# Optimization experiments

Measured on AMD Instinct MI355X. Metric: run time of the kernel, lower is better.

The kernel has to match this reference:

```python
import jax, jax.numpy as jnp
import numpy as np

B, T, C, H = 4, 2048, 1024, 16
HD = C // H  # head_dim = 64


def setup_inputs() -> dict:
    key = jax.random.key(0)
    k1, k2, k3 = jax.random.split(key, 3)
    x = jax.random.normal(k1, (B, T, C), dtype=jnp.float32)
    # nn.Linear weights are [out, in]; we store transposed [in, out] for x @ W
    w_qkv = jax.random.normal(k2, (C, 3 * C), dtype=jnp.float32) * (1.0 / np.sqrt(C))
    w_proj = jax.random.normal(k3, (C, C), dtype=jnp.float32) * (1.0 / np.sqrt(C))
    return {"x": x, "w_qkv": w_qkv, "w_proj": w_proj}


def reference(x, w_qkv, w_proj):
    Bs, Ts, Cs = x.shape
    qkv = x @ w_qkv  # [B,T,3C]
    q, k, v = jnp.split(qkv, 3, axis=-1)

    def split_heads(t):
        return t.reshape(Bs, Ts, H, HD).transpose(0, 2, 1, 3)  # [B,H,T,HD]

    q, k, v = split_heads(q), split_heads(k), split_heads(v)
    scale = 1.0 / np.sqrt(HD)
    scores = jnp.einsum('bhqd,bhkd->bhqk', q, k) * scale  # [B,H,T,T]
    causal = jnp.tril(jnp.ones((Ts, Ts), dtype=bool))
    scores = jnp.where(causal, scores, -jnp.inf)
    weights = jax.nn.softmax(scores, axis=-1)
    out = jnp.einsum('bhqk,bhkd->bhqd', weights, v)  # [B,H,T,HD]
    out = out.transpose(0, 2, 1, 3).reshape(Bs, Ts, Cs)
    return out @ w_proj
```

## Files before the change

kernel.cpp:

```cpp
#include <hip/hip_runtime.h>
#include <stdint.h>


typedef __attribute__((ext_vector_type(8))) short bf16x8;
typedef __attribute__((ext_vector_type(4))) float f32x4;

#define MFMA(a, b, c) __builtin_amdgcn_mfma_f32_16x16x32_bf16((a), (b), (c), 0, 0, 0)

#define NB 4
#define NT 2048
#define NC 1024
#define NH 16
#define HD 64
#define SCALE_Q 0.18033688011112042f

__device__ __forceinline__ short f2bf(float f) {
  union { float fv; uint32_t u; } v; v.fv = f;
  uint32_t u = v.u;
  uint32_t r = (u + 0x7fffu + ((u >> 16) & 1u)) >> 16;
  return (short)(r & 0xffffu);
}

__device__ __forceinline__ void gl_lds16(const void* g, void* l) {
  __builtin_amdgcn_global_load_lds(
      (const __attribute__((address_space(1))) void*)g,
      (__attribute__((address_space(3))) void*)l, 16, 0, 0);
}


__global__ void cast_f32_bf16(const float* __restrict__ src, short* __restrict__ dst, int n8) {
  int i = blockIdx.x * blockDim.x + threadIdx.x;
  if (i >= n8) return;
  const float4* s4 = (const float4*)src;
  float4 a = s4[2 * i], b = s4[2 * i + 1];
  bf16x8 o;
  o[0] = f2bf(a.x); o[1] = f2bf(a.y); o[2] = f2bf(a.z); o[3] = f2bf(a.w);
  o[4] = f2bf(b.x); o[5] = f2bf(b.y); o[6] = f2bf(b.z); o[7] = f2bf(b.w);
  *(bf16x8*)&dst[8 * i] = o;
}

__global__ void transpose_cast(const float* __restrict__ src, short* __restrict__ dst,
                               int R, int Cc) {
  __shared__ float tile[64][65];
  int tid = threadIdx.x;
  int c0 = blockIdx.x * 64;
  int r0 = blockIdx.y * 64;
  int lr = tid >> 4;
  int lc = (tid & 15) * 4;
#pragma unroll
  for (int i = 0; i < 4; i++) {
    int rr = lr + i * 16;
    float4 v = *(const float4*)&src[(size_t)(r0 + rr) * Cc + c0 + lc];
    tile[rr][lc + 0] = v.x; tile[rr][lc + 1] = v.y;
    tile[rr][lc + 2] = v.z; tile[rr][lc + 3] = v.w;
  }
  __syncthreads();
  int oc = tid >> 2;
  int seg = (tid & 3) * 16;
  bf16x8 o0, o1;
#pragma unroll
  for (int u = 0; u < 8; u++) o0[u] = f2bf(tile[seg + u][oc]);
#pragma unroll
  for (int u = 0; u < 8; u++) o1[u] = f2bf(tile[seg + 8 + u][oc]);
  size_t base = (size_t)(c0 + oc) * R + r0 + seg;
  *(bf16x8*)&dst[base] = o0;
  *(bf16x8*)&dst[base + 8] = o1;
}


__global__ __launch_bounds__(256, 2)
void gemm_bt_kernel(const short* __restrict__ A, const short* __restrict__ BT,
                    int N, int K, int nbx, int mode,
                    short* __restrict__ q, short* __restrict__ kk, short* __restrict__ vT,
                    float* __restrict__ f_out) {
  __shared__ short sA[128 * 64];
  __shared__ short sB[128 * 64];
  const int tid = threadIdx.x;
  const int lane = tid & 63;
  const int w = tid >> 6;
  const int quad = lane >> 4;
  const int r = lane & 15;

  const int bid = blockIdx.x;
  const int xcd = bid & 7;
  const int local = bid >> 3;
  const int mloc = local / nbx, nloc = local - mloc * nbx;
  const int bm0 = (xcd * 8 + mloc) * 128;
  const int bn0 = nloc * 128;

  const int wm = (w >> 1) * 64;
  const int wn = (w & 1) * 64;
  const int sel = (mode == 0) ? (bn0 >> 10) : 3;
  const bool swapped = (sel != 2);

  f32x4 acc[4][4];
#pragma unroll
  for (int i = 0; i < 4; i++)
#pragma unroll
    for (int j = 0; j < 4; j++) acc[i][j] = (f32x4){0.f, 0.f, 0.f, 0.f};

  for (int kb = 0; kb < K; kb += 64) {
    __syncthreads();
#pragma unroll
    for (int j2 = 0; j2 < 4; j2++) {
      int idx = (w * 4 + j2) * 64 + lane;
      int row = idx >> 3, ch = idx & 7;
      int g = ch ^ (row & 7);
      gl_lds16(A + (size_t)(bm0 + row) * K + kb + g * 8, (char*)sA + idx * 16);
      gl_lds16(BT + (size_t)(bn0 + row) * K + kb + g * 8, (char*)sB + idx * 16);
    }
    __syncthreads();
#pragma unroll
    for (int c = 0; c < 2; c++) {
      bf16x8 af[4], bfr[4];
#pragma unroll
      for (int i = 0; i < 4; i++) {
        const int sw = ((c << 2) + quad) ^ (r & 7);
        af[i]  = *(const bf16x8*)&sA[(wm + i * 16 + r) * 64 + sw * 8];
        bfr[i] = *(const bf16x8*)&sB[(wn + i * 16 + r) * 64 + sw * 8];
      }
      if (swapped) {
#pragma unroll
        for (int i = 0; i < 4; i++)
#pragma unroll
          for (int j = 0; j < 4; j++)
            acc[i][j] = MFMA(bfr[j], af[i], acc[i][j]);
      } else {
#pragma unroll
        for (int i = 0; i < 4; i++)
#pragma unroll
          for (int j = 0; j < 4; j++)
            acc[i][j] = MFMA(af[i], bfr[j], acc[i][j]);
      }
    }
  }

  if (mode == 1) {
#pragma unroll
    for (int i = 0; i < 4; i++) {
      const int m = bm0 + wm + i * 16 + r;
#pragma unroll
      for (int j = 0; j < 4; j++) {
        const int nf = bn0 + wn + j * 16 + quad * 4;
        *(f32x4*)&f_out[(size_t)m * N + nf] = acc[i][j];
      }
    }
  } else if (sel == 2) {
#pragma unroll
    for (int j = 0; j < 4; j++) {
      const int n = bn0 + wn + j * 16 + r;
      const int d = n & 63, h = (n & 1023) >> 6;
#pragma unroll
      for (int i = 0; i < 4; i++) {
        const int t0 = bm0 + wm + i * 16 + quad * 4;
        const int bh = (t0 >> 11) * NH + h;
        uint32_t p0 = (uint16_t)f2bf(acc[i][j][0]) | ((uint32_t)(uint16_t)f2bf(acc[i][j][1]) << 16);
        uint32_t p1 = (uint16_t)f2bf(acc[i][j][2]) | ((uint32_t)(uint16_t)f2bf(acc[i][j][3]) << 16);
        *(uint2*)&vT[((size_t)bh * HD + d) * NT + (t0 & 2047)] = make_uint2(p0, p1);
      }
    }
  } else {
    short* dst = (sel == 0) ? q : kk;
    const float scl = (sel == 0) ? SCALE_Q : 1.0f;
#pragma unroll
    for (int i = 0; i < 4; i++) {
      const int t = bm0 + wm + i * 16 + r;
      const int bb = (t >> 11) * NH;
      const int tt = t & 2047;
#pragma unroll
      for (int j = 0; j < 4; j++) {
        const int nf = bn0 + wn + j * 16 + quad * 4;
        const int rem = nf & 1023, h = rem >> 6, d0 = rem & 63;
        uint32_t p0 = (uint16_t)f2bf(acc[i][j][0] * scl) | ((uint32_t)(uint16_t)f2bf(acc[i][j][1] * scl) << 16);
        uint32_t p1 = (uint16_t)f2bf(acc[i][j][2] * scl) | ((uint32_t)(uint16_t)f2bf(acc[i][j][3] * scl) << 16);
        *(uint2*)&dst[((size_t)(bb + h) * NT + tt) * HD + d0] = make_uint2(p0, p1);
      }
    }
  }
}


__global__ __launch_bounds__(256, 3)
void attn_kernel(const short* __restrict__ Q, const short* __restrict__ Kg,
                 const short* __restrict__ VT, short* __restrict__ Og) {
  __shared__ short sK[128 * 64];
  __shared__ short sV[64 * 128];
  __shared__ short sP[4][16 * 136];
  const int tid = threadIdx.x;
  const int lane = tid & 63;
  const int w = tid >> 6;
  const int quad = lane >> 4;
  const int r = lane & 15;

  const int n = blockIdx.x;
  const int xcd = n & 7;
  const int slot = n >> 3;
  const int bh = xcd * 8 + (slot & 7);
  const int band = 15 - (slot >> 3);
  const int ntile = band + 1;

  const short* Qb  = Q  + (size_t)bh * NT * HD;
  const short* Kb  = Kg + (size_t)bh * NT * HD;
  const short* VTb = VT + (size_t)bh * HD * NT;

  const int q0 = band * 128 + w * 32;

  bf16x8 bQ[2][2];
#pragma unroll
  for (int mi = 0; mi < 2; mi++) {
    const size_t qrow = ((size_t)q0 + mi * 16 + r) * HD;
    bQ[mi][0] = *(const bf16x8*)&Qb[qrow + quad * 8];
    bQ[mi][1] = *(const bf16x8*)&Qb[qrow + 32 + quad * 8];
  }
  bf16x8 vone;
#pragma unroll
  for (int u = 0; u < 8; u++) vone[u] = (short)0x3F80;

  f32x4 acc[2][4];
  f32x4 lacc[2];
#pragma unroll
  for (int mi = 0; mi < 2; mi++) {
    lacc[mi] = (f32x4){0.f, 0.f, 0.f, 0.f};
#pragma unroll
    for (int dt = 0; dt < 4; dt++) acc[mi][dt] = (f32x4){0.f, 0.f, 0.f, 0.f};
  }

  for (int kt = 0; kt < ntile; kt++) {
    const int kv0 = kt * 128;
    const bool diag = (kt == band);
    __syncthreads();
#pragma unroll
    for (int j = 0; j < 4; j++) {
      int idx = (w * 4 + j) * 64 + lane;
      int krow = idx >> 3, kch = idx & 7;
      int kg = kch ^ (krow & 7);
      gl_lds16(Kb + (size_t)(kv0 + krow) * HD + kg * 8, (char*)sK + idx * 16);
      int vrow = idx >> 4, vch = idx & 15;
      int vg = (vch & 8) | ((vch ^ vrow) & 7);
      gl_lds16(VTb + (size_t)vrow * NT + kv0 + vg * 8, (char*)sV + idx * 16);
    }
    __syncthreads();

    bf16x8 vf[4][4];
#pragma unroll
    for (int dt = 0; dt < 4; dt++)
#pragma unroll
      for (int c = 0; c < 4; c++) {
        int ch = quad + 4 * c;
        int sw = (ch & 8) | ((ch ^ (r & 7)) & 7);
        vf[dt][c] = *(const bf16x8*)&sV[(dt * 16 + r) * 128 + sw * 8];
      }

#pragma unroll
    for (int mi = 0; mi < 2; mi++) {
      const int nts = diag ? (w * 2 + mi + 1) : 8;
#pragma unroll
      for (int nt = 0; nt < 8; nt++) {
        uint32_t pk0 = 0, pk1 = 0;
        if (nt < nts) {
          const int krow = nt * 16 + r;
          const int sw0 = quad ^ (r & 7);
          bf16x8 k0 = *(const bf16x8*)&sK[krow * 64 + sw0 * 8];
          bf16x8 k1 = *(const bf16x8*)&sK[krow * 64 + (sw0 ^ 4) * 8];
          f32x4 st = (f32x4){0.f, 0.f, 0.f, 0.f};
          st = MFMA(k0, bQ[mi][0], st);
          st = MFMA(k1, bQ[mi][1], st);
          if (diag && nt == nts - 1) {
            const int kvb = kv0 + nt * 16 + quad * 4;
            const int qg = q0 + mi * 16 + r;
#pragma unroll
            for (int reg = 0; reg < 4; reg++)
              if (kvb + reg > qg) st[reg] = -1e30f;
          }
          uint32_t b0 = (uint16_t)f2bf(__builtin_amdgcn_exp2f(st[0]));
          uint32_t b1 = (uint16_t)f2bf(__builtin_amdgcn_exp2f(st[1]));
          uint32_t b2 = (uint16_t)f2bf(__builtin_amdgcn_exp2f(st[2]));
          uint32_t b3 = (uint16_t)f2bf(__builtin_amdgcn_exp2f(st[3]));
          pk0 = b0 | (b1 << 16);
          pk1 = b2 | (b3 << 16);
        }
        *(uint2*)&sP[w][r * 136 + nt * 16 + quad * 4] = make_uint2(pk0, pk1);
      }
      __builtin_amdgcn_s_waitcnt(0xc07f);
      bf16x8 aP[4];
#pragma unroll
      for (int c = 0; c < 4; c++)
        aP[c] = *(const bf16x8*)&sP[w][r * 136 + c * 32 + quad * 8];
#pragma unroll
      for (int c = 0; c < 4; c++)
        lacc[mi] = MFMA(aP[c], vone, lacc[mi]);
#pragma unroll
      for (int dt = 0; dt < 4; dt++)
#pragma unroll
        for (int c = 0; c < 4; c++)
          acc[mi][dt] = MFMA(aP[c], vf[dt][c], acc[mi][dt]);
    }
  }

  const int b = bh >> 4, h = bh & 15;
#pragma unroll
  for (int mi = 0; mi < 2; mi++)
#pragma unroll
    for (int reg = 0; reg < 4; reg++) {
      const int trow = q0 + mi * 16 + quad * 4 + reg;
      const float inv = 1.0f / lacc[mi][reg];
      const size_t base = ((size_t)(b * NT + trow)) * NC + h * HD;
#pragma unroll
      for (int dt = 0; dt < 4; dt++)
        Og[base + dt * 16 + r] = f2bf(acc[mi][dt][reg] * inv);
    }
}


extern "C" void kernel_launch(void* const* d_in, const int* in_sizes, int n_in,
                              void* d_out, int out_size, void* d_ws, size_t ws_size,
                              hipStream_t stream) {
  const float* x     = (const float*)d_in[0];
  const float* wqkv  = (const float*)d_in[1];
  const float* wproj = (const float*)d_in[2];
  float* out = (float*)d_out;

  char* ws = (char*)d_ws;
  short* xb  = (short*)(ws + 0);
  short* wqT = (short*)(ws + 16777216);
  short* wpT = (short*)(ws + 23068672);
  short* q   = (short*)(ws + 25165824);
  short* kk  = (short*)(ws + 41943040);
  short* vT  = (short*)(ws + 58720256);
  short* att = (short*)(ws + 75497472);

  cast_f32_bf16<<<4096, 256, 0, stream>>>(x, xb, (NB * NT * NC) / 8);
  transpose_cast<<<dim3(48, 16), 256, 0, stream>>>(wqkv, wqT, NC, 3 * NC);
  transpose_cast<<<dim3(16, 16), 256, 0, stream>>>(wproj, wpT, NC, NC);
  gemm_bt_kernel<<<1536, 256, 0, stream>>>(xb, wqT, 3 * NC, NC, 24, 0, q, kk, vT, nullptr);
  attn_kernel<<<1024, 256, 0, stream>>>(q, kk, vT, att);
  gemm_bt_kernel<<<512, 256, 0, stream>>>(att, wpT, NC, NC, 8, 1, nullptr, nullptr, nullptr, out);
}
```

Before: 259.5 us.

## Pair causal attention bands per block and use cheaper bf16 packing

The attention kernel now runs two query bands per block, a long one (15-pr) and a short one (pr), so every block does the same amount of causal work. This halves the grid to 512 blocks and removes the load imbalance and tail from the triangular band sizes. Separately, bf16 conversion in the GEMM epilogue and the softmax exp path uses a perm-based pack that rounds half away from zero instead of the round-to-nearest-even f2bf, which cuts ALU work. The trade-off is fewer blocks to hide latency with, plus slightly different rounding.

```diff
diff --git a/kernel.cpp b/kernel.cpp
--- a/kernel.cpp
+++ b/kernel.cpp
@@ -19,6 +19,11 @@
   uint32_t u = v.u;
   uint32_t r = (u + 0x7fffu + ((u >> 16) & 1u)) >> 16;
   return (short)(r & 0xffffu);
+}
+
+__device__ __forceinline__ uint32_t pkbf(float a, float b) {
+  union { float f; uint32_t u; } ua, ub; ua.f = a; ub.f = b;
+  return __builtin_amdgcn_perm(ub.u + 0x8000u, ua.u + 0x8000u, 0x07060302u);
 }
 
 __device__ __forceinline__ void gl_lds16(const void* g, void* l) {
@@ -154,9 +159,9 @@
       for (int i = 0; i < 4; i++) {
         const int t0 = bm0 + wm + i * 16 + quad * 4;
         const int bh = (t0 >> 11) * NH + h;
-        uint32_t p0 = (uint16_t)f2bf(acc[i][j][0]) | ((uint32_t)(uint16_t)f2bf(acc[i][j][1]) << 16);
-        uint32_t p1 = (uint16_t)f2bf(acc[i][j][2]) | ((uint32_t)(uint16_t)f2bf(acc[i][j][3]) << 16);
-        *(uint2*)&vT[((size_t)bh * HD + d) * NT + (t0 & 2047)] = make_uint2(p0, p1);
+        uint2 pk = make_uint2(pkbf(acc[i][j][0], acc[i][j][1]),
+                              pkbf(acc[i][j][2], acc[i][j][3]));
+        *(uint2*)&vT[((size_t)bh * HD + d) * NT + (t0 & 2047)] = pk;
       }
     }
   } else {
@@ -171,38 +176,22 @@
       for (int j = 0; j < 4; j++) {
         const int nf = bn0 + wn + j * 16 + quad * 4;
         const int rem = nf & 1023, h = rem >> 6, d0 = rem & 63;
-        uint32_t p0 = (uint16_t)f2bf(acc[i][j][0] * scl) | ((uint32_t)(uint16_t)f2bf(acc[i][j][1] * scl) << 16);
-        uint32_t p1 = (uint16_t)f2bf(acc[i][j][2] * scl) | ((uint32_t)(uint16_t)f2bf(acc[i][j][3] * scl) << 16);
-        *(uint2*)&dst[((size_t)(bb + h) * NT + tt) * HD + d0] = make_uint2(p0, p1);
-      }
-    }
-  }
-}
-
-
-__global__ __launch_bounds__(256, 3)
-void attn_kernel(const short* __restrict__ Q, const short* __restrict__ Kg,
-                 const short* __restrict__ VT, short* __restrict__ Og) {
-  __shared__ short sK[128 * 64];
-  __shared__ short sV[64 * 128];
-  __shared__ short sP[4][16 * 136];
-  const int tid = threadIdx.x;
-  const int lane = tid & 63;
-  const int w = tid >> 6;
+        uint2 pk = make_uint2(pkbf(acc[i][j][0] * scl, acc[i][j][1] * scl),
+                              pkbf(acc[i][j][2] * scl, acc[i][j][3] * scl));
+        *(uint2*)&dst[((size_t)(bb + h) * NT + tt) * HD + d0] = pk;
+      }
+    }
+  }
+}
+
+
+__device__ __forceinline__ void attn_band(
+    const short* __restrict__ Qb, const short* __restrict__ Kb,
+    const short* __restrict__ VTb, short* __restrict__ Og,
+    short* __restrict__ sK, short* __restrict__ sV, short* __restrict__ sPw,
+    const int band, const int bh, const int w, const int lane) {
   const int quad = lane >> 4;
   const int r = lane & 15;
-
-  const int n = blockIdx.x;
-  const int xcd = n & 7;
-  const int slot = n >> 3;
-  const int bh = xcd * 8 + (slot & 7);
-  const int band = 15 - (slot >> 3);
-  const int ntile = band + 1;
-
-  const short* Qb  = Q  + (size_t)bh * NT * HD;
-  const short* Kb  = Kg + (size_t)bh * NT * HD;
-  const short* VTb = VT + (size_t)bh * HD * NT;
-
   const int q0 = band * 128 + w * 32;
 
   bf16x8 bQ[2][2];
@@ -225,7 +214,7 @@
     for (int dt = 0; dt < 4; dt++) acc[mi][dt] = (f32x4){0.f, 0.f, 0.f, 0.f};
   }
 
-  for (int kt = 0; kt < ntile; kt++) {
+  for (int kt = 0; kt <= band; kt++) {
     const int kv0 = kt * 128;
     const bool diag = (kt == band);
     __syncthreads();
@@ -256,7 +245,7 @@
       const int nts = diag ? (w * 2 + mi + 1) : 8;
 #pragma unroll
       for (int nt = 0; nt < 8; nt++) {
-        uint32_t pk0 = 0, pk1 = 0;
+        uint2 pk = make_uint2(0u, 0u);
         if (nt < nts) {
           const int krow = nt * 16 + r;
           const int sw0 = quad ^ (r & 7);
@@ -272,20 +261,16 @@
             for (int reg = 0; reg < 4; reg++)
               if (kvb + reg > qg) st[reg] = -1e30f;
           }
-          uint32_t b0 = (uint16_t)f2bf(__builtin_amdgcn_exp2f(st[0]));
-          uint32_t b1 = (uint16_t)f2bf(__builtin_amdgcn_exp2f(st[1]));
-          uint32_t b2 = (uint16_t)f2bf(__builtin_amdgcn_exp2f(st[2]));
-          uint32_t b3 = (uint16_t)f2bf(__builtin_amdgcn_exp2f(st[3]));
-          pk0 = b0 | (b1 << 16);
-          pk1 = b2 | (b3 << 16);
+          pk.x = pkbf(__builtin_amdgcn_exp2f(st[0]), __builtin_amdgcn_exp2f(st[1]));
+          pk.y = pkbf(__builtin_amdgcn_exp2f(st[2]), __builtin_amdgcn_exp2f(st[3]));
         }
-        *(uint2*)&sP[w][r * 136 + nt * 16 + quad * 4] = make_uint2(pk0, pk1);
+        *(uint2*)&sPw[r * 136 + nt * 16 + quad * 4] = pk;
       }
       __builtin_amdgcn_s_waitcnt(0xc07f);
       bf16x8 aP[4];
 #pragma unroll
       for (int c = 0; c < 4; c++)
-        aP[c] = *(const bf16x8*)&sP[w][r * 136 + c * 32 + quad * 8];
+        aP[c] = *(const bf16x8*)&sPw[r * 136 + c * 32 + quad * 8];
 #pragma unroll
       for (int c = 0; c < 4; c++)
         lacc[mi] = MFMA(aP[c], vone, lacc[mi]);
@@ -309,6 +294,30 @@
       for (int dt = 0; dt < 4; dt++)
         Og[base + dt * 16 + r] = f2bf(acc[mi][dt][reg] * inv);
     }
+}
+
+__global__ __launch_bounds__(256, 3)
+void attn_kernel(const short* __restrict__ Q, const short* __restrict__ Kg,
+                 const short* __restrict__ VT, short* __restrict__ Og) {
+  __shared__ short sK[128 * 64];
+  __shared__ short sV[64 * 128];
+  __shared__ short sP[4][16 * 136];
+  const int tid = threadIdx.x;
+  const int lane = tid & 63;
+  const int w = tid >> 6;
+
+  const int n = blockIdx.x;
+  const int xcd = n & 7;
+  const int slot = n >> 3;
+  const int bh = xcd * 8 + (slot & 7);
+  const int pr = slot >> 3;
+
+  const short* Qb  = Q  + (size_t)bh * NT * HD;
+  const short* Kb  = Kg + (size_t)bh * NT * HD;
+  const short* VTb = VT + (size_t)bh * HD * NT;
+
+  attn_band(Qb, Kb, VTb, Og, sK, sV, &sP[w][0], 15 - pr, bh, w, lane);
+  attn_band(Qb, Kb, VTb, Og, sK, sV, &sP[w][0], pr, bh, w, lane);
 }
 
 
@@ -333,6 +342,6 @@
   transpose_cast<<<dim3(48, 16), 256, 0, stream>>>(wqkv, wqT, NC, 3 * NC);
   transpose_cast<<<dim3(16, 16), 256, 0, stream>>>(wproj, wpT, NC, NC);
   gemm_bt_kernel<<<1536, 256, 0, stream>>>(xb, wqT, 3 * NC, NC, 24, 0, q, kk, vT, nullptr);
-  attn_kernel<<<1024, 256, 0, stream>>>(q, kk, vT, att);
+  attn_kernel<<<512, 256, 0, stream>>>(q, kk, vT, att);
   gemm_bt_kernel<<<512, 256, 0, stream>>>(att, wpT, NC, NC, 8, 1, nullptr, nullptr, nullptr, out);
 }
```

Measured after the change: 300.0 us. +15.6%, slower.
